# Kernel tuning notes

Measured on AMD Instinct MI355X. Metric: run time of the kernel, lower is better.

## Reference

```python
import jax, jax.numpy as jnp
import numpy as np

# Problem constants (NumberOfUsers=8, TimeLength=128)
E = 1024                 # EigneVectorSize = NumberOfUsers * TimeLength
K = 20                   # NumberOfEigenFun
NOUT = K * (2 * E + 1)   # NumberOfOutputs = 40980
VLOC = K + K * E         # VmatrixLocation
PENALTY = 0.01


def setup_inputs() -> dict:
    key = jax.random.key(0)
    k1, k2, k3 = jax.random.split(key, 3)
    B = 32
    nnOutput = jax.random.normal(k1, (B, 2 * NOUT), dtype=jnp.float32)
    kern_real = jax.random.normal(k2, (B, E, E), dtype=jnp.float32)
    kern_imag = jax.random.normal(k3, (B, E, E), dtype=jnp.float32)
    return {"nnOutput": nnOutput, "kern_real": kern_real,
            "kern_imag": kern_imag, "batch_Size": B}


def _orthogonality(M, batch_Size):
    # M: [B, E, K] complex. Original triple loop computes
    # sum_{b} sum_{j<k} |sum_e M[b,e,j]*M[b,e,k]| / B  (NO conjugation)
    G = jnp.einsum('bej,bek->bjk', M, M)           # [B, K, K] complex Gram (no conj)
    mask = jnp.triu(jnp.ones((K, K), dtype=bool), k=1)
    return jnp.sum(jnp.where(mask[None], jnp.abs(G), 0.0)) / batch_Size


def reference(nnOutput, kern_real, kern_imag, batch_Size):
    B = nnOutput.shape[0]
    c = jax.lax.complex(nnOutput[:, :NOUT], nnOutput[:, NOUT:2 * NOUT])  # [B, NOUT] complex64
    d = c[:, :K]                                   # [B, K] diagonal entries
    U = c[:, K:VLOC].reshape(B, E, K)              # [B, E, K]
    V = c[:, VLOC:NOUT].reshape(B, E, K)           # [B, E, K]

    obj1 = _orthogonality(U, batch_Size)
    obj2 = _orthogonality(V, batch_Size)

    # kernels_pred = U @ diag(d) @ V^T  (fold the diagonal into U; no diag_embed)
    kernels_pred = jnp.einsum('bek,bk,bfk->bef', U, d, V)  # [B, E, E] complex

    tk = jax.lax.complex(kern_real, kern_imag)     # train_kernals_2d
    diff = tk - kernels_pred
    # torch.norm(x, 2)**2 on complex = sum |x|^2
    num = jnp.sum(diff.real ** 2 + diff.imag ** 2)
    den = jnp.sum(kern_real ** 2 + kern_imag ** 2)
    mse_norm = num / den

    loss = mse_norm + PENALTY * obj1 + PENALTY * obj2
    return (loss, obj1, obj2)
```

## Files before the change

kernel.cpp:

```cpp
#include <hip/hip_runtime.h>

#define E 1024
#define KK 20
#define NOUT 40980
#define VLOC 20500
#define SROW (2*NOUT)
#define NPAIR 190


__global__ __launch_bounds__(256) void gram_kernel(const float* __restrict__ nn,
                                                   float* __restrict__ ws) {
    __shared__ float2 sM[128 * 21];
    __shared__ float red[4];
    int bw = blockIdx.x, b = bw >> 1, which = bw & 1;
    const float* baseR = nn + (size_t)b * SROW + (which ? VLOC : KK);
    const float* baseI = baseR + NOUT;
    int t = threadIdx.x;
    int j = 0, kq = 1;
    if (t < NPAIR) {
        int p = t, cnt = KK - 1;
        while (p >= cnt) { p -= cnt; j++; cnt--; }
        kq = j + 1 + p;
    }
    float gr = 0.f, gi = 0.f;
    float rR[10], rI[10];
    #pragma unroll
    for (int i = 0; i < 10; i++) { int idx = t + i * 256; rR[i] = baseR[idx]; rI[i] = baseI[idx]; }
    for (int c = 0; c < 8; c++) {
        #pragma unroll
        for (int i = 0; i < 10; i++) {
            int idx = t + i * 256;
            sM[idx + idx / KK] = make_float2(rR[i], rI[i]);
        }
        __syncthreads();
        if (c < 7) {
            const float* nR = baseR + (c + 1) * 2560;
            const float* nI = baseI + (c + 1) * 2560;
            #pragma unroll
            for (int i = 0; i < 10; i++) { int idx = t + i * 256; rR[i] = nR[idx]; rI[i] = nI[idx]; }
        }
        if (t < NPAIR) {
            #pragma unroll 8
            for (int e = 0; e < 128; e++) {
                float2 a = sM[e * 21 + j];
                float2 cc = sM[e * 21 + kq];
                gr += a.x * cc.x - a.y * cc.y;
                gi += a.x * cc.y + a.y * cc.x;
            }
        }
        __syncthreads();
    }
    float m = (t < NPAIR) ? sqrtf(gr * gr + gi * gi) : 0.f;
    #pragma unroll
    for (int off = 32; off > 0; off >>= 1) m += __shfl_down(m, off, 64);
    if ((t & 63) == 0) red[t >> 6] = m;
    __syncthreads();
    if (t == 0) ws[bw] = red[0] + red[1] + red[2] + red[3];
}

__global__ __launch_bounds__(256) void main_kernel(const float* __restrict__ nn,
                                                   const float* __restrict__ krn_r,
                                                   const float* __restrict__ krn_i,
                                                   float* __restrict__ ws) {
    __shared__ float2 sW[10 * 128];
    __shared__ float2 sV[10 * 128];
    __shared__ float redN[4], redD[4];
    int b = blockIdx.z;
    int e0 = blockIdx.y * 128;
    int f0 = blockIdx.x * 128;
    const float* nb = nn + (size_t)b * SROW;
    int t = threadIdx.x;
    int fe = (t & 15) * 8;
    int te = (t >> 4) * 8;

    float pr[8][8], pi[8][8];
    #pragma unroll
    for (int i = 0; i < 8; i++)
        #pragma unroll
        for (int q = 0; q < 8; q++) { pr[i][q] = 0.f; pi[i][q] = 0.f; }

    #pragma unroll 1
    for (int h = 0; h < 2; h++) {
        int k0 = h * 10;
        if (h) __syncthreads();
        for (int idx = t; idx < 640; idx += 256) {
            int e = idx & 127, kp = idx >> 7;
            int k = k0 + kp * 2;
            const float* pu = nb + KK + (size_t)(e0 + e) * KK + k;
            float2 ur = *(const float2*)pu;
            float2 ui = *(const float2*)(pu + NOUT);
            const float* pv = nb + VLOC + (size_t)(f0 + e) * KK + k;
            float2 vr = *(const float2*)pv;
            float2 vi = *(const float2*)(pv + NOUT);
            float dr0 = nb[k], di0 = nb[NOUT + k];
            float dr1 = nb[k + 1], di1 = nb[NOUT + k + 1];
            sW[(kp * 2) * 128 + e]     = make_float2(ur.x * dr0 - ui.x * di0, ur.x * di0 + ui.x * dr0);
            sW[(kp * 2 + 1) * 128 + e] = make_float2(ur.y * dr1 - ui.y * di1, ur.y * di1 + ui.y * dr1);
            sV[(kp * 2) * 128 + e]     = make_float2(vr.x, vi.x);
            sV[(kp * 2 + 1) * 128 + e] = make_float2(vr.y, vi.y);
        }
        __syncthreads();
        #pragma unroll 2
        for (int k = 0; k < 10; k++) {
            const float4* wp = (const float4*)(sW + k * 128 + te);
            const float4* vp = (const float4*)(sV + k * 128 + fe);
            float4 wA = wp[0], wB = wp[1], wC = wp[2], wD = wp[3];
            float4 vA = vp[0], vB = vp[1], vC = vp[2], vD = vp[3];
            float2 w[8] = {{wA.x,wA.y},{wA.z,wA.w},{wB.x,wB.y},{wB.z,wB.w},
                           {wC.x,wC.y},{wC.z,wC.w},{wD.x,wD.y},{wD.z,wD.w}};
            float2 v[8] = {{vA.x,vA.y},{vA.z,vA.w},{vB.x,vB.y},{vB.z,vB.w},
                           {vC.x,vC.y},{vC.z,vC.w},{vD.x,vD.y},{vD.z,vD.w}};
            #pragma unroll
            for (int i = 0; i < 8; i++)
                #pragma unroll
                for (int q = 0; q < 8; q++) {
                    pr[i][q] += w[i].x * v[q].x - w[i].y * v[q].y;
                    pi[i][q] += w[i].x * v[q].y + w[i].y * v[q].x;
                }
        }
    }

    float num = 0.f, den = 0.f;
    size_t base = ((size_t)b * E + (size_t)(e0 + te)) * E + (size_t)(f0 + fe);
    #pragma unroll
    for (int i = 0; i < 8; i++) {
        const float* rp = krn_r + base + (size_t)i * E;
        const float* qp = krn_i + base + (size_t)i * E;
        float4 r0 = *(const float4*)rp;
        float4 r1 = *(const float4*)(rp + 4);
        float4 q0 = *(const float4*)qp;
        float4 q1 = *(const float4*)(qp + 4);
        float rr[8] = {r0.x,r0.y,r0.z,r0.w,r1.x,r1.y,r1.z,r1.w};
        float qq[8] = {q0.x,q0.y,q0.z,q0.w,q1.x,q1.y,q1.z,q1.w};
        #pragma unroll
        for (int q = 0; q < 8; q++) {
            float dr = rr[q] - pr[i][q];
            float di = qq[q] - pi[i][q];
            num += dr * dr + di * di;
            den += rr[q] * rr[q] + qq[q] * qq[q];
        }
    }
    #pragma unroll
    for (int off = 32; off > 0; off >>= 1) {
        num += __shfl_down(num, off, 64);
        den += __shfl_down(den, off, 64);
    }
    if ((t & 63) == 0) { redN[t >> 6] = num; redD[t >> 6] = den; }
    __syncthreads();
    if (t == 0) {
        int bid = ((int)blockIdx.z * 8 + (int)blockIdx.y) * 8 + (int)blockIdx.x;
        int moff = (int)gridDim.z * 2 + bid * 2;
        ws[moff]     = redN[0] + redN[1] + redN[2] + redN[3];
        ws[moff + 1] = redD[0] + redD[1] + redD[2] + redD[3];
    }
}

__global__ __launch_bounds__(256) void fin_kernel(const float* __restrict__ ws,
                                                  const int* __restrict__ bsz,
                                                  float* __restrict__ out, int B) {
    __shared__ float acc[16];
    int t = threadIdx.x;
    float num = 0.f, den = 0.f, sU = 0.f, sV = 0.f;
    int moff = B * 2;
    int nmain = B * 64;
    for (int i = t; i < nmain; i += 256) {
        num += ws[moff + 2 * i];
        den += ws[moff + 2 * i + 1];
    }
    for (int i = t; i < B * 2; i += 256) {
        float g = ws[i];
        if (i & 1) sV += g; else sU += g;
    }
    #pragma unroll
    for (int off = 32; off > 0; off >>= 1) {
        num += __shfl_down(num, off, 64);
        den += __shfl_down(den, off, 64);
        sU  += __shfl_down(sU, off, 64);
        sV  += __shfl_down(sV, off, 64);
    }
    if ((t & 63) == 0) {
        int w = t >> 6;
        acc[w * 4 + 0] = num; acc[w * 4 + 1] = den;
        acc[w * 4 + 2] = sU;  acc[w * 4 + 3] = sV;
    }
    __syncthreads();
    if (t == 0) {
        num = acc[0] + acc[4] + acc[8]  + acc[12];
        den = acc[1] + acc[5] + acc[9]  + acc[13];
        sU  = acc[2] + acc[6] + acc[10] + acc[14];
        sV  = acc[3] + acc[7] + acc[11] + acc[15];
        float Bf = (float)bsz[0];
        float o1 = sU / Bf, o2 = sV / Bf;
        out[0] = num / den + 0.01f * (o1 + o2);
        out[1] = o1;
        out[2] = o2;
    }
}

extern "C" void kernel_launch(void* const* d_in, const int* in_sizes, int n_in,
                              void* d_out, int out_size, void* d_ws, size_t ws_size,
                              hipStream_t stream) {
    const float* nn = (const float*)d_in[0];
    const float* kr = (const float*)d_in[1];
    const float* ki = (const float*)d_in[2];
    const int* bsz = (const int*)d_in[3];
    float* ws = (float*)d_ws;
    float* out = (float*)d_out;
    int B = in_sizes[0] / SROW;

    hipLaunchKernelGGL(gram_kernel, dim3(B * 2), dim3(256), 0, stream, nn, ws);
    hipLaunchKernelGGL(main_kernel, dim3(E / 128, E / 128, B), dim3(256), 0, stream,
                       nn, kr, ki, ws);
    hipLaunchKernelGGL(fin_kernel, dim3(1), dim3(256), 0, stream, ws, bsz, out, B);
}
```

Measured before the change: 349.2 us.

## Stage all K in LDS once, swizzle V layout, prefetch kernel tiles under compute

The main kernel now loads all 20 eigenfunction columns of W=U*diag(d) and V into shared memory in a single pass, removing the second load phase and its barrier. The V tile is stored with an XOR swizzle so that the strided float4 reads by the 16 column-threads avoid LDS bank conflicts. The global loads of the first rows of the target kernel are issued between the two halves of the K loop, and the remaining rows are loaded two at a time while earlier rows are consumed, so memory latency overlaps the FMA work. In exchange, LDS use doubles and register pressure rises because of the in-flight prefetch buffers.

```diff
diff --git a/kernel.cpp b/kernel.cpp
--- a/kernel.cpp
+++ b/kernel.cpp
@@ -62,8 +62,8 @@
                                                    const float* __restrict__ krn_r,
                                                    const float* __restrict__ krn_i,
                                                    float* __restrict__ ws) {
-    __shared__ float2 sW[10 * 128];
-    __shared__ float2 sV[10 * 128];
+    __shared__ float2 sW[KK * 128];
+    __shared__ float2 sV[KK * 128];
     __shared__ float redN[4], redD[4];
     int b = blockIdx.z;
     int e0 = blockIdx.y * 128;
@@ -73,73 +73,108 @@
     int fe = (t & 15) * 8;
     int te = (t >> 4) * 8;
 
+    int i4 = (t & 15) * 4;
+    int voff0, voff1, voff2, voff3;
+    { int F, Fs;
+      F = i4 + 0; Fs = F ^ ((F >> 3) & 7); voff0 = Fs << 1;
+      F = i4 + 1; Fs = F ^ ((F >> 3) & 7); voff1 = Fs << 1;
+      F = i4 + 2; Fs = F ^ ((F >> 3) & 7); voff2 = Fs << 1;
+      F = i4 + 3; Fs = F ^ ((F >> 3) & 7); voff3 = Fs << 1; }
+
+    for (int idx = t; idx < 1280; idx += 256) {
+        int e = idx & 127, kp = idx >> 7;
+        int k = kp * 2;
+        const float* pu = nb + KK + (size_t)(e0 + e) * KK + k;
+        float2 ur = *(const float2*)pu;
+        float2 ui = *(const float2*)(pu + NOUT);
+        const float* pv = nb + VLOC + (size_t)(f0 + e) * KK + k;
+        float2 vr = *(const float2*)pv;
+        float2 vi = *(const float2*)(pv + NOUT);
+        float dr0 = nb[k], di0 = nb[NOUT + k];
+        float dr1 = nb[k + 1], di1 = nb[NOUT + k + 1];
+        int F = e >> 1;
+        int es = ((F ^ ((F >> 3) & 7)) << 1) | (e & 1);
+        sW[k * 128 + e]        = make_float2(ur.x * dr0 - ui.x * di0, ur.x * di0 + ui.x * dr0);
+        sW[(k + 1) * 128 + e]  = make_float2(ur.y * dr1 - ui.y * di1, ur.y * di1 + ui.y * dr1);
+        sV[k * 128 + es]       = make_float2(vr.x, vi.x);
+        sV[(k + 1) * 128 + es] = make_float2(vr.y, vi.y);
+    }
+    __syncthreads();
+
     float pr[8][8], pi[8][8];
     #pragma unroll
     for (int i = 0; i < 8; i++)
         #pragma unroll
         for (int q = 0; q < 8; q++) { pr[i][q] = 0.f; pi[i][q] = 0.f; }
 
-    #pragma unroll 1
-    for (int h = 0; h < 2; h++) {
-        int k0 = h * 10;
-        if (h) __syncthreads();
-        for (int idx = t; idx < 640; idx += 256) {
-            int e = idx & 127, kp = idx >> 7;
-            int k = k0 + kp * 2;
-            const float* pu = nb + KK + (size_t)(e0 + e) * KK + k;
-            float2 ur = *(const float2*)pu;
-            float2 ui = *(const float2*)(pu + NOUT);
-            const float* pv = nb + VLOC + (size_t)(f0 + e) * KK + k;
-            float2 vr = *(const float2*)pv;
-            float2 vi = *(const float2*)(pv + NOUT);
-            float dr0 = nb[k], di0 = nb[NOUT + k];
-            float dr1 = nb[k + 1], di1 = nb[NOUT + k + 1];
-            sW[(kp * 2) * 128 + e]     = make_float2(ur.x * dr0 - ui.x * di0, ur.x * di0 + ui.x * dr0);
-            sW[(kp * 2 + 1) * 128 + e] = make_float2(ur.y * dr1 - ui.y * di1, ur.y * di1 + ui.y * dr1);
-            sV[(kp * 2) * 128 + e]     = make_float2(vr.x, vi.x);
-            sV[(kp * 2 + 1) * 128 + e] = make_float2(vr.y, vi.y);
-        }
-        __syncthreads();
-        #pragma unroll 2
-        for (int k = 0; k < 10; k++) {
-            const float4* wp = (const float4*)(sW + k * 128 + te);
-            const float4* vp = (const float4*)(sV + k * 128 + fe);
-            float4 wA = wp[0], wB = wp[1], wC = wp[2], wD = wp[3];
-            float4 vA = vp[0], vB = vp[1], vC = vp[2], vD = vp[3];
-            float2 w[8] = {{wA.x,wA.y},{wA.z,wA.w},{wB.x,wB.y},{wB.z,wB.w},
-                           {wC.x,wC.y},{wC.z,wC.w},{wD.x,wD.y},{wD.z,wD.w}};
-            float2 v[8] = {{vA.x,vA.y},{vA.z,vA.w},{vB.x,vB.y},{vB.z,vB.w},
-                           {vC.x,vC.y},{vC.z,vC.w},{vD.x,vD.y},{vD.z,vD.w}};
-            #pragma unroll
-            for (int i = 0; i < 8; i++)
-                #pragma unroll
-                for (int q = 0; q < 8; q++) {
-                    pr[i][q] += w[i].x * v[q].x - w[i].y * v[q].y;
-                    pi[i][q] += w[i].x * v[q].y + w[i].y * v[q].x;
-                }
-        }
-    }
+#define KSTEP(k) { \
+        const float2* sWr = sW + (k) * 128; \
+        const float2* sVr = sV + (k) * 128; \
+        float4 wA = *(const float4*)(sWr + te);     \
+        float4 wB = *(const float4*)(sWr + te + 2); \
+        float4 wC = *(const float4*)(sWr + te + 4); \
+        float4 wD = *(const float4*)(sWr + te + 6); \
+        float4 vA = *(const float4*)(sVr + voff0);  \
+        float4 vB = *(const float4*)(sVr + voff1);  \
+        float4 vC = *(const float4*)(sVr + voff2);  \
+        float4 vD = *(const float4*)(sVr + voff3);  \
+        float2 w[8] = {{wA.x,wA.y},{wA.z,wA.w},{wB.x,wB.y},{wB.z,wB.w}, \
+                       {wC.x,wC.y},{wC.z,wC.w},{wD.x,wD.y},{wD.z,wD.w}}; \
+        float2 v[8] = {{vA.x,vA.y},{vA.z,vA.w},{vB.x,vB.y},{vB.z,vB.w}, \
+                       {vC.x,vC.y},{vC.z,vC.w},{vD.x,vD.y},{vD.z,vD.w}}; \
+        _Pragma("unroll") \
+        for (int i = 0; i < 8; i++) \
+            _Pragma("unroll") \
+            for (int q = 0; q < 8; q++) { \
+                pr[i][q] += w[i].x * v[q].x - w[i].y * v[q].y; \
+                pi[i][q] += w[i].x * v[q].y + w[i].y * v[q].x; \
+            } }
+
+    #pragma unroll 2
+    for (int k = 0; k < 10; k++) KSTEP(k)
+
+    size_t base = ((size_t)b * E + (size_t)(e0 + te)) * E + (size_t)(f0 + fe);
+    const float* rp = krn_r + base;
+    const float* qp = krn_i + base;
+#define LDROW(R0,R1,Q0,Q1,I) { \
+        const float* _r = rp + (size_t)(I) * E; \
+        const float* _q = qp + (size_t)(I) * E; \
+        R0 = *(const float4*)_r;  R1 = *(const float4*)(_r + 4); \
+        Q0 = *(const float4*)_q;  Q1 = *(const float4*)(_q + 4); }
+    float4 Ar0, Ar1, Aq0, Aq1, Br0, Br1, Bq0, Bq1;
+    float4 Cr0, Cr1, Cq0, Cq1, Dr0, Dr1, Dq0, Dq1;
+    LDROW(Ar0, Ar1, Aq0, Aq1, 0)
+    LDROW(Br0, Br1, Bq0, Bq1, 1)
+
+    #pragma unroll 2
+    for (int k = 10; k < 20; k++) KSTEP(k)
 
     float num = 0.f, den = 0.f;
-    size_t base = ((size_t)b * E + (size_t)(e0 + te)) * E + (size_t)(f0 + fe);
-    #pragma unroll
-    for (int i = 0; i < 8; i++) {
-        const float* rp = krn_r + base + (size_t)i * E;
-        const float* qp = krn_i + base + (size_t)i * E;
-        float4 r0 = *(const float4*)rp;
-        float4 r1 = *(const float4*)(rp + 4);
-        float4 q0 = *(const float4*)qp;
-        float4 q1 = *(const float4*)(qp + 4);
-        float rr[8] = {r0.x,r0.y,r0.z,r0.w,r1.x,r1.y,r1.z,r1.w};
-        float qq[8] = {q0.x,q0.y,q0.z,q0.w,q1.x,q1.y,q1.z,q1.w};
-        #pragma unroll
-        for (int q = 0; q < 8; q++) {
-            float dr = rr[q] - pr[i][q];
-            float di = qq[q] - pi[i][q];
-            num += dr * dr + di * di;
-            den += rr[q] * rr[q] + qq[q] * qq[q];
-        }
-    }
+#define CONS(R0,R1,Q0,Q1,I) { \
+        float rr[8] = {R0.x,R0.y,R0.z,R0.w,R1.x,R1.y,R1.z,R1.w}; \
+        float qq[8] = {Q0.x,Q0.y,Q0.z,Q0.w,Q1.x,Q1.y,Q1.z,Q1.w}; \
+        _Pragma("unroll") \
+        for (int q = 0; q < 8; q++) { \
+            float dr = rr[q] - pr[I][q]; \
+            float di = qq[q] - pi[I][q]; \
+            num += dr * dr + di * di; \
+            den += rr[q] * rr[q] + qq[q] * qq[q]; } }
+
+    LDROW(Cr0, Cr1, Cq0, Cq1, 2)
+    LDROW(Dr0, Dr1, Dq0, Dq1, 3)
+    CONS(Ar0, Ar1, Aq0, Aq1, 0)
+    CONS(Br0, Br1, Bq0, Bq1, 1)
+    LDROW(Ar0, Ar1, Aq0, Aq1, 4)
+    LDROW(Br0, Br1, Bq0, Bq1, 5)
+    CONS(Cr0, Cr1, Cq0, Cq1, 2)
+    CONS(Dr0, Dr1, Dq0, Dq1, 3)
+    LDROW(Cr0, Cr1, Cq0, Cq1, 6)
+    LDROW(Dr0, Dr1, Dq0, Dq1, 7)
+    CONS(Ar0, Ar1, Aq0, Aq1, 4)
+    CONS(Br0, Br1, Bq0, Bq1, 5)
+    CONS(Cr0, Cr1, Cq0, Cq1, 6)
+    CONS(Dr0, Dr1, Dq0, Dq1, 7)
+
     #pragma unroll
     for (int off = 32; off > 0; off >>= 1) {
         num += __shfl_down(num, off, 64);
@@ -160,7 +195,7 @@
                                                   float* __restrict__ out, int B) {
     __shared__ float acc[16];
     int t = threadIdx.x;
-    float num = 0.f, den = 0.f, sU = 0.f, sV = 0.f;
+    float num = 0.f, den = 0.f, sU = 0.f, sV2 = 0.f;
     int moff = B * 2;
     int nmain = B * 64;
     for (int i = t; i < nmain; i += 256) {
@@ -169,28 +204,28 @@
     }
     for (int i = t; i < B * 2; i += 256) {
         float g = ws[i];
-        if (i & 1) sV += g; else sU += g;
+        if (i & 1) sV2 += g; else sU += g;
     }
     #pragma unroll
     for (int off = 32; off > 0; off >>= 1) {
         num += __shfl_down(num, off, 64);
         den += __shfl_down(den, off, 64);
         sU  += __shfl_down(sU, off, 64);
-        sV  += __shfl_down(sV, off, 64);
+        sV2 += __shfl_down(sV2, off, 64);
     }
     if ((t & 63) == 0) {
         int w = t >> 6;
         acc[w * 4 + 0] = num; acc[w * 4 + 1] = den;
-        acc[w * 4 + 2] = sU;  acc[w * 4 + 3] = sV;
+        acc[w * 4 + 2] = sU;  acc[w * 4 + 3] = sV2;
     }
     __syncthreads();
     if (t == 0) {
         num = acc[0] + acc[4] + acc[8]  + acc[12];
         den = acc[1] + acc[5] + acc[9]  + acc[13];
         sU  = acc[2] + acc[6] + acc[10] + acc[14];
-        sV  = acc[3] + acc[7] + acc[11] + acc[15];
+        sV2 = acc[3] + acc[7] + acc[11] + acc[15];
         float Bf = (float)bsz[0];
-        float o1 = sU / Bf, o2 = sV / Bf;
+        float o1 = sU / Bf, o2 = sV2 / Bf;
         out[0] = num / den + 0.01f * (o1 + o2);
         out[1] = o1;
         out[2] = o2;
```

After: 338.0 us. 1.03x faster.
